# Kernel optimization log

Hardware: AMD Instinct MI355X
Metric: run time of the kernel (lower is better)

Reference implementation:

```python
import jax, jax.numpy as jnp
import numpy as np

B, T, IN, H = 4096, 128, 768, 256


def setup_inputs() -> dict:
    key = jax.random.key(0)
    ks = jax.random.split(key, 5)
    s1 = 1.0 / np.sqrt(IN)
    s2 = 1.0 / np.sqrt(H)
    return {
        "x": jax.random.normal(ks[0], (B, IN), jnp.float32),
        "W1": jax.random.normal(ks[1], (T, IN, H), jnp.float32) * s1,
        "b1": jnp.zeros((T, H), jnp.float32),
        "W2": jax.random.normal(ks[2], (T, H, H), jnp.float32) * s2,
        "b2": jnp.zeros((T, H), jnp.float32),
        "W3": jax.random.normal(ks[3], (T, H), jnp.float32) * s2,
        "b3": jnp.zeros((T,), jnp.float32),
    }


def reference(x, W1, b1, W2, b2, W3, b3):
    # Per-task 3-layer MLP, vectorized over tasks. Dropout is eval-mode (identity).
    h = jax.nn.relu(jnp.einsum('bi,tih->bth', x, W1) + b1)          # [B, T, H]
    h = jax.nn.relu(jnp.einsum('bth,thk->btk', h, W2) + b2)         # [B, T, H]
    out = jnp.einsum('bth,th->bt', h, W3) + b3                      # [B, T]
    return out
```

## Files before the change

### kernel.cpp

```cpp
#include <hip/hip_runtime.h>
#include <cstdint>
#include <cstddef>

#define B_   4096
#define T_   128
#define IN_  768
#define H_   256
#define BM_  256
#define KC1  (IN_ / 32)
#define NC2  16

typedef __bf16 bf16_t;
typedef bf16_t bf16x8 __attribute__((ext_vector_type(8)));
typedef bf16_t bf16x4 __attribute__((ext_vector_type(4)));
typedef float  floatx16 __attribute__((ext_vector_type(16)));

#define MFMA32(a, b, c) __builtin_amdgcn_mfma_f32_32x32x16_bf16((a), (b), (c), 0, 0, 0)

__device__ __forceinline__ void gl_lds16(const bf16_t* g, bf16_t* l) {
    __builtin_amdgcn_global_load_lds(
        (const __attribute__((address_space(1))) void*)g,
        (__attribute__((address_space(3))) void*)l, 16, 0, 0);
}

template <int N>
__device__ __forceinline__ void vmwait() {
    asm volatile("s_waitcnt vmcnt(%0)" :: "i"(N) : "memory");
}
__device__ __forceinline__ void wg_barrier() {
    asm volatile("" ::: "memory");
    __builtin_amdgcn_s_barrier();
    asm volatile("" ::: "memory");
}

__global__ __launch_bounds__(256)
void tile_all(const float* __restrict__ x, const float* __restrict__ W1,
              const float* __restrict__ W2, bf16_t* __restrict__ xt,
              bf16_t* __restrict__ w1t, bf16_t* __restrict__ w2t) {
    const int b   = blockIdx.x;
    const int tid = threadIdx.x;
    if (b < T_ * KC1 + T_ * 8) {
        const float* src; bf16_t* dst; int t, kc, K, KC;
        if (b < T_ * KC1) { t = b / KC1; kc = b - t * KC1; K = IN_; KC = KC1; src = W1; dst = w1t; }
        else { int bb = b - T_ * KC1; t = bb >> 3; kc = bb & 7; K = H_; KC = 8; src = W2; dst = w2t; }
        const int kq = tid >> 6, h4 = (tid & 63) * 4;
        const float* s = src + ((size_t)t * K + kc * 32 + kq * 8) * H_ + h4;
        float r[8][4];
#pragma unroll
        for (int e = 0; e < 8; ++e) {
            float4 v = *(const float4*)(s + (size_t)e * H_);
            r[e][0] = v.x; r[e][1] = v.y; r[e][2] = v.z; r[e][3] = v.w;
        }
        bf16_t* d = dst + (((size_t)(t * KC + kc) * 4 + kq) * H_ + h4) * 8;
#pragma unroll
        for (int c = 0; c < 4; ++c) {
            bf16x8 v;
#pragma unroll
            for (int e = 0; e < 8; ++e) v[e] = (bf16_t)r[e][c];
            *(bf16x8*)(d + c * 8) = v;
        }
    } else {
        const int bb = b - (T_ * KC1 + T_ * 8);
        const int mb = bb / KC1, kc = bb - mb * KC1;
        const int r = tid >> 3, c = tid & 7;
#pragma unroll
        for (int it = 0; it < 4; ++it) {
            const int m = it * 32 + r;
            float4 v = *(const float4*)(x + ((size_t)(mb * 128 + m)) * IN_ + kc * 32 + c * 4);
            bf16x4 o; o[0] = (bf16_t)v.x; o[1] = (bf16_t)v.y; o[2] = (bf16_t)v.z; o[3] = (bf16_t)v.w;
            *(bf16x4*)(xt + ((size_t)(mb * KC1 + kc) * 4 + (c >> 1)) * 1024 + m * 8 + (c & 1) * 4) = o;
        }
    }
}

__global__ __launch_bounds__(512, 1)
void mtmlp_fused5(const bf16_t* __restrict__ xt, const bf16_t* __restrict__ w1t,
                  const float* __restrict__ b1, const bf16_t* __restrict__ w2t,
                  const float* __restrict__ b2, const float* __restrict__ W3,
                  const float* __restrict__ b3, float* __restrict__ out) {
    const int L    = blockIdx.x;
    const int xcd  = L & 7;
    const int slot = L >> 3;
    const int t    = xcd * 16 + (slot >> 4);
    const int mblk = slot & 15;
    const int m0   = mblk * BM_;
    const int mb0  = mblk * 2;

    const int tid  = threadIdx.x;
    const int lane = tid & 63;
    const int wid  = tid >> 6;
    const int wm   = wid >> 2;
    const int wn   = wid & 3;
    const int ln31 = lane & 31;
    const int hi   = lane >> 5;

    __shared__ __align__(16) bf16_t hbuf[BM_ * H_];
    __shared__ __align__(16) bf16_t wt2[3 * 4096];
    float* w3s = (float*)wt2;

    floatx16 acc[4][2];
#pragma unroll
    for (int i = 0; i < 4; ++i)
#pragma unroll
        for (int j = 0; j < 2; ++j)
#pragma unroll
            for (int e = 0; e < 16; ++e) acc[i][j][e] = 0.0f;

    const bf16_t* w1base = w1t + (size_t)t * KC1 * 8192;
    const bf16_t* x0base = xt + (size_t)mb0 * KC1 * 4096;
    const bf16_t* x1base = xt + (size_t)(mb0 + 1) * KC1 * 4096;

    auto stage1 = [&](int sl, int kc) {
        bf16_t* buf = hbuf + sl * 16384;
        const bf16_t* ws = w1base + (size_t)kc * 8192;
        gl_lds16(ws + tid * 8,        buf + tid * 8);
        gl_lds16(ws + 4096 + tid * 8, buf + 4096 + tid * 8);
        gl_lds16(x0base + (size_t)kc * 4096 + tid * 8, buf + 8192 + tid * 8);
        gl_lds16(x1base + (size_t)kc * 4096 + tid * 8, buf + 12288 + tid * 8);
    };
    auto comp1 = [&](int sl) {
        const bf16_t* buf = hbuf + sl * 16384;
#pragma unroll
        for (int s = 0; s < 2; ++s) {
            const int kq = s * 2 + hi;
            bf16x8 A[4], Bf[2];
#pragma unroll
            for (int i = 0; i < 4; ++i)
                A[i] = *(const bf16x8*)(buf + (size_t)(kq * H_ + wm * 128 + i * 32 + ln31) * 8);
#pragma unroll
            for (int j = 0; j < 2; ++j) {
                const int mm = wn * 64 + j * 32 + ln31;
                Bf[j] = *(const bf16x8*)(buf + 8192 + (mm >> 7) * 4096 +
                                         (size_t)(kq * 128 + (mm & 127)) * 8);
            }
#pragma unroll
            for (int i = 0; i < 4; ++i)
#pragma unroll
                for (int j = 0; j < 2; ++j) acc[i][j] = MFMA32(A[i], Bf[j], acc[i][j]);
        }
    };

    stage1(0, 0); stage1(1, 1); stage1(2, 2);
    for (int kc = 0; kc <= KC1 - 4; ++kc) {
        vmwait<8>();
        wg_barrier();
        stage1((kc + 3) & 3, kc + 3);
        comp1(kc & 3);
    }
    vmwait<8>(); wg_barrier(); comp1((KC1 - 3) & 3);
    vmwait<4>(); wg_barrier(); comp1((KC1 - 2) & 3);
    vmwait<0>(); wg_barrier(); comp1((KC1 - 1) & 3);

    __syncthreads();

    const bf16_t* w2base = w2t + (size_t)t * 32 * 2048;
    auto stage2 = [&](int sl, int c) {
        gl_lds16(w2base + (size_t)c * 4096 + tid * 8, wt2 + sl * 4096 + tid * 8);
    };
    stage2(0, 0); stage2(1, 1);

#pragma unroll
    for (int i = 0; i < 4; ++i) {
#pragma unroll
        for (int g = 0; g < 4; ++g) {
            const int h0 = wm * 128 + i * 32 + g * 8 + 4 * hi;
            float4 bias = *(const float4*)(b1 + t * H_ + h0);
            const int blk = h0 >> 3;
#pragma unroll
            for (int j = 0; j < 2; ++j) {
                const int mm = wn * 64 + j * 32 + ln31;
                bf16x4 o;
                o[0] = (bf16_t)fmaxf(acc[i][j][4 * g + 0] + bias.x, 0.0f);
                o[1] = (bf16_t)fmaxf(acc[i][j][4 * g + 1] + bias.y, 0.0f);
                o[2] = (bf16_t)fmaxf(acc[i][j][4 * g + 2] + bias.z, 0.0f);
                o[3] = (bf16_t)fmaxf(acc[i][j][4 * g + 3] + bias.w, 0.0f);
                *(bf16x4*)(hbuf + (size_t)(blk * BM_ + mm) * 8 + 4 * hi) = o;
            }
        }
    }

#pragma unroll
    for (int i = 0; i < 4; ++i)
#pragma unroll
        for (int j = 0; j < 2; ++j)
#pragma unroll
            for (int e = 0; e < 16; ++e) acc[i][j][e] = 0.0f;

    __syncthreads();

    auto comp2 = [&](int sl, int c) {
        const bf16_t* buf = wt2 + sl * 4096;
        bf16x8 A[4], Bf[2];
#pragma unroll
        for (int i = 0; i < 4; ++i)
            A[i] = *(const bf16x8*)(buf + (size_t)(hi * H_ + wm * 128 + i * 32 + ln31) * 8);
        const int blk = c * 2 + hi;
#pragma unroll
        for (int j = 0; j < 2; ++j) {
            const int mm = wn * 64 + j * 32 + ln31;
            Bf[j] = *(const bf16x8*)(hbuf + (size_t)(blk * BM_ + mm) * 8);
        }
#pragma unroll
        for (int i = 0; i < 4; ++i)
#pragma unroll
            for (int j = 0; j < 2; ++j) acc[i][j] = MFMA32(A[i], Bf[j], acc[i][j]);
    };

    {
        int sl = 0, sp = 2;
        for (int c = 0; c <= NC2 - 3; ++c) {
            vmwait<1>();
            wg_barrier();
            stage2(sp, c + 2);
            comp2(sl, c);
            sl = (sl == 2) ? 0 : sl + 1;
            sp = (sp == 2) ? 0 : sp + 1;
        }
    }
    vmwait<1>(); wg_barrier(); comp2((NC2 - 2) % 3, NC2 - 2);
    vmwait<0>(); wg_barrier(); comp2((NC2 - 1) % 3, NC2 - 1);

    __syncthreads();

    if (tid < H_) w3s[tid] = W3[t * H_ + tid];
#pragma unroll
    for (int i = 0; i < 4; ++i) {
#pragma unroll
        for (int g = 0; g < 4; ++g) {
            const int h0 = wm * 128 + i * 32 + g * 8 + 4 * hi;
            float4 bias = *(const float4*)(b2 + t * H_ + h0);
            const int blk = h0 >> 3;
#pragma unroll
            for (int j = 0; j < 2; ++j) {
                const int mm = wn * 64 + j * 32 + ln31;
                bf16x4 o;
                o[0] = (bf16_t)fmaxf(acc[i][j][4 * g + 0] + bias.x, 0.0f);
                o[1] = (bf16_t)fmaxf(acc[i][j][4 * g + 1] + bias.y, 0.0f);
                o[2] = (bf16_t)fmaxf(acc[i][j][4 * g + 2] + bias.z, 0.0f);
                o[3] = (bf16_t)fmaxf(acc[i][j][4 * g + 3] + bias.w, 0.0f);
                *(bf16x4*)(hbuf + (size_t)(blk * BM_ + mm) * 8 + 4 * hi) = o;
            }
        }
    }
    __syncthreads();

    {
        const int m = tid >> 1, seg = tid & 1;
        float sum = 0.0f;
#pragma unroll
        for (int b = 0; b < 16; ++b) {
            const int blk = seg * 16 + b;
            const bf16x8 v = *(const bf16x8*)(hbuf + (size_t)(blk * BM_ + m) * 8);
            const float* w = w3s + blk * 8;
#pragma unroll
            for (int e = 0; e < 8; ++e) sum += (float)v[e] * w[e];
        }
        sum += __shfl_xor(sum, 1);
        if (seg == 0) out[(size_t)(m0 + m) * T_ + t] = sum + b3[t];
    }
}

extern "C" void kernel_launch(void* const* d_in, const int* in_sizes, int n_in,
                              void* d_out, int out_size, void* d_ws, size_t ws_size,
                              hipStream_t stream) {
    const float* x  = (const float*)d_in[0];
    const float* W1 = (const float*)d_in[1];
    const float* b1 = (const float*)d_in[2];
    const float* W2 = (const float*)d_in[3];
    const float* b2 = (const float*)d_in[4];
    const float* W3 = (const float*)d_in[5];
    const float* b3 = (const float*)d_in[6];
    float* out = (float*)d_out;

    const size_t nx  = (size_t)B_ * IN_;
    const size_t nw1 = (size_t)T_ * IN_ * H_;

    bf16_t* xt  = (bf16_t*)d_ws;
    bf16_t* w1t = xt + nx;
    bf16_t* w2t = w1t + nw1;

    tile_all<<<dim3(T_ * KC1 + T_ * 8 + 32 * KC1), 256, 0, stream>>>(x, W1, W2, xt, w1t, w2t);
    mtmlp_fused5<<<dim3(2048), 512, 0, stream>>>(xt, w1t, b1, w2t, b2, W3, b3, out);
}
```

Baseline: 485.7 us.

## Halve row tile, stream X fragments from global into registers, double-buffer weights via LDS

The fused MLP kernel drops from 256 to 128 rows per block, runs 256 threads at two blocks per CU, and launches twice as many blocks. Instead of async global-to-LDS copies of both operands, weight chunks go through registers into a 2-slot LDS ring. The X fragments are loaded directly from global memory into MFMA operand registers. The aim is more resident waves for latency hiding and less LDS traffic, at the cost of reading each weight chunk twice as often and relying on register-prefetch latency hiding.

```diff
diff --git a/kernel.cpp b/kernel.cpp
--- a/kernel.cpp
+++ b/kernel.cpp
@@ -6,9 +6,10 @@
 #define T_   128
 #define IN_  768
 #define H_   256
-#define BM_  256
+#define BM_  128
 #define KC1  (IN_ / 32)
-#define NC2  16
+#define NS1  48
+#define NS2  16
 
 typedef __bf16 bf16_t;
 typedef bf16_t bf16x8 __attribute__((ext_vector_type(8)));
@@ -17,18 +18,8 @@
 
 #define MFMA32(a, b, c) __builtin_amdgcn_mfma_f32_32x32x16_bf16((a), (b), (c), 0, 0, 0)
 
-__device__ __forceinline__ void gl_lds16(const bf16_t* g, bf16_t* l) {
-    __builtin_amdgcn_global_load_lds(
-        (const __attribute__((address_space(1))) void*)g,
-        (__attribute__((address_space(3))) void*)l, 16, 0, 0);
-}
-
-template <int N>
-__device__ __forceinline__ void vmwait() {
-    asm volatile("s_waitcnt vmcnt(%0)" :: "i"(N) : "memory");
-}
-__device__ __forceinline__ void wg_barrier() {
-    asm volatile("" ::: "memory");
+__device__ __forceinline__ void lgkm0_barrier() {
+    asm volatile("s_waitcnt lgkmcnt(0)" ::: "memory");
     __builtin_amdgcn_s_barrier();
     asm volatile("" ::: "memory");
 }
@@ -73,158 +64,173 @@
     }
 }
 
-__global__ __launch_bounds__(512, 1)
-void mtmlp_fused5(const bf16_t* __restrict__ xt, const bf16_t* __restrict__ w1t,
+__global__ __launch_bounds__(256, 2)
+void mtmlp_fused6(const bf16_t* __restrict__ xt, const bf16_t* __restrict__ w1t,
                   const float* __restrict__ b1, const bf16_t* __restrict__ w2t,
                   const float* __restrict__ b2, const float* __restrict__ W3,
                   const float* __restrict__ b3, float* __restrict__ out) {
     const int L    = blockIdx.x;
     const int xcd  = L & 7;
-    const int slot = L >> 3;
-    const int t    = xcd * 16 + (slot >> 4);
-    const int mblk = slot & 15;
+    const int idx  = L >> 3;
+    const int t    = xcd * 16 + (idx >> 5);
+    const int mblk = idx & 31;
     const int m0   = mblk * BM_;
-    const int mb0  = mblk * 2;
 
     const int tid  = threadIdx.x;
     const int lane = tid & 63;
     const int wid  = tid >> 6;
-    const int wm   = wid >> 2;
-    const int wn   = wid & 3;
+    const int wm   = wid & 1;
+    const int wn   = wid >> 1;
     const int ln31 = lane & 31;
     const int hi   = lane >> 5;
 
     __shared__ __align__(16) bf16_t hbuf[BM_ * H_];
-    __shared__ __align__(16) bf16_t wt2[3 * 4096];
-    float* w3s = (float*)wt2;
-
-    floatx16 acc[4][2];
-#pragma unroll
-    for (int i = 0; i < 4; ++i)
+    __shared__ __align__(16) bf16_t wring[2 * 4096];
+    float* w3s = (float*)wring;
+
+    floatx16 acc[2][2];
+#pragma unroll
+    for (int i = 0; i < 2; ++i)
 #pragma unroll
         for (int j = 0; j < 2; ++j)
 #pragma unroll
             for (int e = 0; e < 16; ++e) acc[i][j][e] = 0.0f;
-
-    const bf16_t* w1base = w1t + (size_t)t * KC1 * 8192;
-    const bf16_t* x0base = xt + (size_t)mb0 * KC1 * 4096;
-    const bf16_t* x1base = xt + (size_t)(mb0 + 1) * KC1 * 4096;
-
-    auto stage1 = [&](int sl, int kc) {
-        bf16_t* buf = hbuf + sl * 16384;
-        const bf16_t* ws = w1base + (size_t)kc * 8192;
-        gl_lds16(ws + tid * 8,        buf + tid * 8);
-        gl_lds16(ws + 4096 + tid * 8, buf + 4096 + tid * 8);
-        gl_lds16(x0base + (size_t)kc * 4096 + tid * 8, buf + 8192 + tid * 8);
-        gl_lds16(x1base + (size_t)kc * 4096 + tid * 8, buf + 12288 + tid * 8);
-    };
-    auto comp1 = [&](int sl) {
-        const bf16_t* buf = hbuf + sl * 16384;
-#pragma unroll
-        for (int s = 0; s < 2; ++s) {
-            const int kq = s * 2 + hi;
-            bf16x8 A[4], Bf[2];
-#pragma unroll
-            for (int i = 0; i < 4; ++i)
-                A[i] = *(const bf16x8*)(buf + (size_t)(kq * H_ + wm * 128 + i * 32 + ln31) * 8);
-#pragma unroll
-            for (int j = 0; j < 2; ++j) {
-                const int mm = wn * 64 + j * 32 + ln31;
-                Bf[j] = *(const bf16x8*)(buf + 8192 + (mm >> 7) * 4096 +
-                                         (size_t)(kq * 128 + (mm & 127)) * 8);
+    floatx16 acc2[2][2];
+#pragma unroll
+    for (int i = 0; i < 2; ++i)
+#pragma unroll
+        for (int j = 0; j < 2; ++j)
+#pragma unroll
+            for (int e = 0; e < 16; ++e) acc2[i][j][e] = 0.0f;
+
+    const bf16_t* w1base = w1t + (size_t)t * NS1 * 4096;
+    const bf16_t* w2base = w2t + (size_t)t * NS2 * 4096;
+    const bf16_t* xbase  = xt + (size_t)mblk * KC1 * 4096;
+    const int woff = tid * 16;
+    const int xoff = (wn * 64 + ln31) * 8;
+
+    bf16x8 wrA[2], wrB[2], xcur[2], xnxt[2];
+
+    auto loadW = [&](bf16x8* r, const bf16_t* base, int c) {
+        const bf16_t* p = base + (size_t)c * 4096 + woff;
+        r[0] = *(const bf16x8*)(p);
+        r[1] = *(const bf16x8*)(p + 8);
+    };
+    auto writeW = [&](const bf16x8* r, int sl) {
+        bf16_t* p = wring + sl * 4096 + woff;
+        *(bf16x8*)(p)     = r[0];
+        *(bf16x8*)(p + 8) = r[1];
+    };
+    auto loadX = [&](bf16x8* r, int c) {
+        const bf16_t* p = xbase + ((size_t)((c >> 1) * 4 + (c & 1) * 2 + hi)) * 1024 + xoff;
+        r[0] = *(const bf16x8*)(p);
+        r[1] = *(const bf16x8*)(p + 256);
+    };
+    auto comp = [&](const bf16x8* xf, int sl) {
+        const bf16_t* buf = wring + sl * 4096;
+        bf16x8 A0 = *(const bf16x8*)(buf + (size_t)(hi * 256 + wm * 128 + 0 * 32 + ln31) * 8);
+        bf16x8 A1 = *(const bf16x8*)(buf + (size_t)(hi * 256 + wm * 128 + 1 * 32 + ln31) * 8);
+        bf16x8 A2 = *(const bf16x8*)(buf + (size_t)(hi * 256 + wm * 128 + 2 * 32 + ln31) * 8);
+        bf16x8 A3 = *(const bf16x8*)(buf + (size_t)(hi * 256 + wm * 128 + 3 * 32 + ln31) * 8);
+#pragma unroll
+        for (int j = 0; j < 2; ++j) {
+            acc[0][j]  = MFMA32(A0, xf[j], acc[0][j]);
+            acc[1][j]  = MFMA32(A1, xf[j], acc[1][j]);
+            acc2[0][j] = MFMA32(A2, xf[j], acc2[0][j]);
+            acc2[1][j] = MFMA32(A3, xf[j], acc2[1][j]);
+        }
+    };
+
+    loadW(wrA, w1base, 0); loadW(wrB, w1base, 1); loadX(xcur, 0);
+    writeW(wrA, 0);
+    lgkm0_barrier();
+
+    for (int c = 0; c < NS1 - 2; c += 2) {
+        writeW(wrB, 1);
+        loadW(wrA, w1base, c + 2);
+        loadX(xnxt, c + 1);
+        comp(xcur, 0);
+        lgkm0_barrier();
+        writeW(wrA, 0);
+        loadW(wrB, w1base, c + 3);
+        loadX(xcur, c + 2);
+        comp(xnxt, 1);
+        lgkm0_barrier();
+    }
+    writeW(wrB, 1);
+    loadX(xnxt, 47);
+    loadW(wrA, w2base, 0);
+    loadW(wrB, w2base, 1);
+    comp(xcur, 0);
+    lgkm0_barrier();
+    comp(xnxt, 1);
+
+    {
+        const floatx16* accp[4] = {&acc[0][0], nullptr, nullptr, nullptr};
+#pragma unroll
+        for (int i = 0; i < 4; ++i) {
+            const floatx16* a0 = (i < 2) ? &acc[i][0] : &acc2[i - 2][0];
+#pragma unroll
+            for (int g = 0; g < 4; ++g) {
+                const int h0 = wm * 128 + i * 32 + g * 8 + 4 * hi;
+                float4 bias = *(const float4*)(b1 + t * H_ + h0);
+                const int blk = h0 >> 3;
+#pragma unroll
+                for (int j = 0; j < 2; ++j) {
+                    const int mm = wn * 64 + j * 32 + ln31;
+                    const floatx16& a = a0[j];
+                    bf16x4 o;
+                    o[0] = (bf16_t)fmaxf(a[4 * g + 0] + bias.x, 0.0f);
+                    o[1] = (bf16_t)fmaxf(a[4 * g + 1] + bias.y, 0.0f);
+                    o[2] = (bf16_t)fmaxf(a[4 * g + 2] + bias.z, 0.0f);
+                    o[3] = (bf16_t)fmaxf(a[4 * g + 3] + bias.w, 0.0f);
+                    *(bf16x4*)(hbuf + (size_t)(blk * BM_ + mm) * 8 + 4 * hi) = o;
+                }
             }
-#pragma unroll
-            for (int i = 0; i < 4; ++i)
-#pragma unroll
-                for (int j = 0; j < 2; ++j) acc[i][j] = MFMA32(A[i], Bf[j], acc[i][j]);
-        }
-    };
-
-    stage1(0, 0); stage1(1, 1); stage1(2, 2);
-    for (int kc = 0; kc <= KC1 - 4; ++kc) {
-        vmwait<8>();
-        wg_barrier();
-        stage1((kc + 3) & 3, kc + 3);
-        comp1(kc & 3);
-    }
-    vmwait<8>(); wg_barrier(); comp1((KC1 - 3) & 3);
-    vmwait<4>(); wg_barrier(); comp1((KC1 - 2) & 3);
-    vmwait<0>(); wg_barrier(); comp1((KC1 - 1) & 3);
-
-    __syncthreads();
-
-    const bf16_t* w2base = w2t + (size_t)t * 32 * 2048;
-    auto stage2 = [&](int sl, int c) {
-        gl_lds16(w2base + (size_t)c * 4096 + tid * 8, wt2 + sl * 4096 + tid * 8);
-    };
-    stage2(0, 0); stage2(1, 1);
-
-#pragma unroll
-    for (int i = 0; i < 4; ++i) {
-#pragma unroll
-        for (int g = 0; g < 4; ++g) {
-            const int h0 = wm * 128 + i * 32 + g * 8 + 4 * hi;
-            float4 bias = *(const float4*)(b1 + t * H_ + h0);
-            const int blk = h0 >> 3;
-#pragma unroll
-            for (int j = 0; j < 2; ++j) {
-                const int mm = wn * 64 + j * 32 + ln31;
-                bf16x4 o;
-                o[0] = (bf16_t)fmaxf(acc[i][j][4 * g + 0] + bias.x, 0.0f);
-                o[1] = (bf16_t)fmaxf(acc[i][j][4 * g + 1] + bias.y, 0.0f);
-                o[2] = (bf16_t)fmaxf(acc[i][j][4 * g + 2] + bias.z, 0.0f);
-                o[3] = (bf16_t)fmaxf(acc[i][j][4 * g + 3] + bias.w, 0.0f);
-                *(bf16x4*)(hbuf + (size_t)(blk * BM_ + mm) * 8 + 4 * hi) = o;
-            }
-        }
-    }
-
-#pragma unroll
-    for (int i = 0; i < 4; ++i)
+        }
+        (void)accp;
+    }
+#pragma unroll
+    for (int i = 0; i < 2; ++i)
 #pragma unroll
         for (int j = 0; j < 2; ++j)
 #pragma unroll
-            for (int e = 0; e < 16; ++e) acc[i][j][e] = 0.0f;
-
-    __syncthreads();
-
-    auto comp2 = [&](int sl, int c) {
-        const bf16_t* buf = wt2 + sl * 4096;
-        bf16x8 A[4], Bf[2];
-#pragma unroll
-        for (int i = 0; i < 4; ++i)
-            A[i] = *(const bf16x8*)(buf + (size_t)(hi * H_ + wm * 128 + i * 32 + ln31) * 8);
+            for (int e = 0; e < 16; ++e) { acc[i][j][e] = 0.0f; acc2[i][j][e] = 0.0f; }
+
+    writeW(wrA, 0);
+    lgkm0_barrier();
+
+    auto comp2 = [&](int c, int sl) {
+        bf16x8 Bf[2];
         const int blk = c * 2 + hi;
 #pragma unroll
         for (int j = 0; j < 2; ++j) {
             const int mm = wn * 64 + j * 32 + ln31;
             Bf[j] = *(const bf16x8*)(hbuf + (size_t)(blk * BM_ + mm) * 8);
         }
-#pragma unroll
-        for (int i = 0; i < 4; ++i)
-#pragma unroll
-            for (int j = 0; j < 2; ++j) acc[i][j] = MFMA32(A[i], Bf[j], acc[i][j]);
-    };
-
-    {
-        int sl = 0, sp = 2;
-        for (int c = 0; c <= NC2 - 3; ++c) {
-            vmwait<1>();
-            wg_barrier();
-            stage2(sp, c + 2);
-            comp2(sl, c);
-            sl = (sl == 2) ? 0 : sl + 1;
-            sp = (sp == 2) ? 0 : sp + 1;
-        }
-    }
-    vmwait<1>(); wg_barrier(); comp2((NC2 - 2) % 3, NC2 - 2);
-    vmwait<0>(); wg_barrier(); comp2((NC2 - 1) % 3, NC2 - 1);
-
-    __syncthreads();
-
+        comp(Bf, sl);
+    };
+
+    for (int c = 0; c < NS2 - 2; c += 2) {
+        writeW(wrB, 1);
+        loadW(wrA, w2base, c + 2);
+        comp2(c, 0);
+        lgkm0_barrier();
+        writeW(wrA, 0);
+        loadW(wrB, w2base, c + 3);
+        comp2(c + 1, 1);
+        lgkm0_barrier();
+    }
+    writeW(wrB, 1);
+    comp2(14, 0);
+    lgkm0_barrier();
     if (tid < H_) w3s[tid] = W3[t * H_ + tid];
+    comp2(15, 1);
+    lgkm0_barrier();
+
 #pragma unroll
     for (int i = 0; i < 4; ++i) {
+        const floatx16* a0 = (i < 2) ? &acc[i][0] : &acc2[i - 2][0];
 #pragma unroll
         for (int g = 0; g < 4; ++g) {
             const int h0 = wm * 128 + i * 32 + g * 8 + 4 * hi;
@@ -233,16 +239,17 @@
 #pragma unroll
             for (int j = 0; j < 2; ++j) {
                 const int mm = wn * 64 + j * 32 + ln31;
+                const floatx16& a = a0[j];
                 bf16x4 o;
-                o[0] = (bf16_t)fmaxf(acc[i][j][4 * g + 0] + bias.x, 0.0f);
-                o[1] = (bf16_t)fmaxf(acc[i][j][4 * g + 1] + bias.y, 0.0f);
-                o[2] = (bf16_t)fmaxf(acc[i][j][4 * g + 2] + bias.z, 0.0f);
-                o[3] = (bf16_t)fmaxf(acc[i][j][4 * g + 3] + bias.w, 0.0f);
+                o[0] = (bf16_t)fmaxf(a[4 * g + 0] + bias.x, 0.0f);
+                o[1] = (bf16_t)fmaxf(a[4 * g + 1] + bias.y, 0.0f);
+                o[2] = (bf16_t)fmaxf(a[4 * g + 2] + bias.z, 0.0f);
+                o[3] = (bf16_t)fmaxf(a[4 * g + 3] + bias.w, 0.0f);
                 *(bf16x4*)(hbuf + (size_t)(blk * BM_ + mm) * 8 + 4 * hi) = o;
             }
         }
     }
-    __syncthreads();
+    lgkm0_barrier();
 
     {
         const int m = tid >> 1, seg = tid & 1;
@@ -280,5 +287,5 @@
     bf16_t* w2t = w1t + nw1;
 
     tile_all<<<dim3(T_ * KC1 + T_ * 8 + 32 * KC1), 256, 0, stream>>>(x, W1, W2, xt, w1t, w2t);
-    mtmlp_fused5<<<dim3(2048), 512, 0, stream>>>(xt, w1t, b1, w2t, b2, W3, b3, out);
-}
+    mtmlp_fused6<<<dim3(4096), 256, 0, stream>>>(xt, w1t, b1, w2t, b2, W3, b3, out);
+}
```

New measurement: 474.8 us. -2.2%, faster.
